# Kernel optimization log

Measured on AMD Instinct MI355X. Metric: run time of the kernel, lower is better.

## Reference

```python
import jax, jax.numpy as jnp
import numpy as np

DIM = 256
NUM_HEADS = 8
SAMPLE_RATIO = 4
B, H, W = 8, 32, 32
HEAD_DIM = DIM // NUM_HEADS
SCALE = HEAD_DIM ** (-0.5)


def conv1x1(x, w, b):
    # x: [B,C,H,W], w: [O,C], b: [O]  (1x1 conv == per-pixel channel matmul)
    return jnp.einsum('bchw,oc->bohw', x, w) + b[None, :, None, None]


def setup_inputs() -> dict:
    key = jax.random.key(0)
    ks = jax.random.split(key, 16)
    s = 0.02
    x = jax.random.normal(ks[0], (B, DIM, H, W), dtype=jnp.float32)
    # gumbel noise for the two gumbel-softmax gates (sampled once, fed as input)
    u_q = jax.random.uniform(ks[1], (B, SAMPLE_RATIO, H, W), minval=1e-6, maxval=1.0 - 1e-6)
    u_k = jax.random.uniform(ks[2], (B, SAMPLE_RATIO, H, W), minval=1e-6, maxval=1.0 - 1e-6)
    g_q = -jnp.log(-jnp.log(u_q))
    g_k = -jnp.log(-jnp.log(u_k))
    return {
        'x': x,
        'g_q': g_q,
        'g_k': g_k,
        'Wsq': jax.random.normal(ks[3], (SAMPLE_RATIO, DIM)) * s,
        'bsq': jnp.zeros((SAMPLE_RATIO,), jnp.float32),
        'Wsk': jax.random.normal(ks[4], (SAMPLE_RATIO, DIM)) * s,
        'bsk': jnp.zeros((SAMPLE_RATIO,), jnp.float32),
        'Wq': jax.random.normal(ks[5], (DIM, DIM)) * s,
        'bq': jnp.zeros((DIM,), jnp.float32),
        'Wk': jax.random.normal(ks[6], (DIM, DIM)) * s,
        'bk': jnp.zeros((DIM,), jnp.float32),
        'Wv': jax.random.normal(ks[7], (DIM, DIM)) * s,
        'bv': jnp.zeros((DIM,), jnp.float32),
        'Wp': jax.random.normal(ks[8], (DIM, DIM)) * s,
        'bp': jnp.zeros((DIM,), jnp.float32),
    }


def reference(x, g_q, g_k, Wsq, bsq, Wsk, bsk, Wq, bq, Wk, bk, Wv, bv, Wp, bp):
    Bn, C, Hh, Ww = x.shape
    N = Hh * Ww
    # gumbel-softmax (soft, tau=1) gates; keep channel 0 only
    sample_q = jax.nn.softmax(conv1x1(x, Wsq, bsq) + g_q, axis=1)[:, :1]   # [B,1,H,W]
    sample_k = jax.nn.softmax(conv1x1(x, Wsk, bsk) + g_k, axis=1)[:, :1]

    q = (sample_q * conv1x1(x, Wq, bq)).reshape(Bn, NUM_HEADS, HEAD_DIM, N)
    k = (sample_k * conv1x1(x, Wk, bk)).reshape(Bn, NUM_HEADS, HEAD_DIM, N)
    v_full = conv1x1(x, Wv, bv)                                            # shortcut [B,C,H,W]
    v = v_full.reshape(Bn, NUM_HEADS, HEAD_DIM, N)

    # dense attention: scores [B,h,N,N]
    attn = jax.nn.softmax(jnp.einsum('bhdn,bhdm->bhnm', q * SCALE, k), axis=-1)
    out = jnp.einsum('bhnm,bhdm->bhdn', attn, v).reshape(Bn, C, Hh, Ww)

    gated = sample_q * out + (1.0 - sample_q) * v_full
    return conv1x1(gated, Wp, bp)
```

## Files before the change

### kernel.cpp

```cpp
#include <hip/hip_runtime.h>
#include <hip/hip_bf16.h>

typedef __hip_bfloat16 bf16;
typedef __attribute__((ext_vector_type(8))) short short8;
typedef __attribute__((ext_vector_type(4))) short sh4;
typedef __attribute__((ext_vector_type(4))) float f32x4;

static __device__ __forceinline__ float bf2f(bf16 h) { return __bfloat162float(h); }
static __device__ __forceinline__ short f2bfs(float f) {
    bf16 h = __float2bfloat16(f);
    return *reinterpret_cast<short*>(&h);
}
static __device__ __forceinline__ short8 cvt8(float4 a, float4 b) {
    short8 o;
    o[0] = f2bfs(a.x); o[1] = f2bfs(a.y); o[2] = f2bfs(a.z); o[3] = f2bfs(a.w);
    o[4] = f2bfs(b.x); o[5] = f2bfs(b.y); o[6] = f2bfs(b.z); o[7] = f2bfs(b.w);
    return o;
}

constexpr int Bn = 8;
constexpr int C  = 256;
constexpr int N  = 1024;
constexpr int NH = 8;
constexpr int HD = 32;
constexpr int TS = 264;
constexpr float SCALE = 0.17677669529663687f;

__global__ __launch_bounds__(256) void k_prep(
    const float* __restrict__ Wq, const float* __restrict__ Wk,
    const float* __restrict__ Wv, const float* __restrict__ Wp,
    bf16* __restrict__ Wb)
{
    const int tid = threadIdx.x;
    const int mat = blockIdx.x >> 2, seg = blockIdx.x & 3;
    const float* src = (mat == 0) ? Wq : (mat == 1) ? Wk : (mat == 2) ? Wv : Wp;
    short* dst = reinterpret_cast<short*>(Wb) + (size_t)mat * 256 * 256;
#pragma unroll
    for (int i = 0; i < 16; ++i) {
        int f4 = seg * 4096 + i * 256 + tid;
        float4 v = reinterpret_cast<const float4*>(src)[f4];
        sh4 o;
        o[0] = f2bfs(v.x); o[1] = f2bfs(v.y); o[2] = f2bfs(v.z); o[3] = f2bfs(v.w);
        *reinterpret_cast<sh4*>(dst + (size_t)f4 * 4) = o;
    }
}

__global__ __launch_bounds__(256) void k_fused5(
    const float* __restrict__ x, const float* __restrict__ gq, const float* __restrict__ gk,
    const float* __restrict__ Wsq, const float* __restrict__ bsq,
    const float* __restrict__ Wsk, const float* __restrict__ bsk,
    const bf16* __restrict__ Wb,
    const float* __restrict__ bq, const float* __restrict__ bk, const float* __restrict__ bv,
    bf16* __restrict__ qo, bf16* __restrict__ ko, bf16* __restrict__ vo,
    float* __restrict__ sqg)
{
    __shared__ short T[64 * TS];
    __shared__ float sq_lds[64];
    __shared__ float sk_lds[64];

    const int tid  = threadIdx.x;
    const int wave = tid >> 6;
    const int lane = tid & 63;
    const int col  = lane & 15;
    const int quad = lane >> 4;

    const int b    = blockIdx.x >> 6;
    const int rest = blockIdx.x & 63;
    const int n0   = (rest >> 2) * 64;
    const int mq   = rest & 3;

    {
        const float* xp = x + (size_t)b * C * N + n0;
        const int row = tid >> 4;
        const int f   = tid & 15;
#pragma unroll
        for (int p = 0; p < 16; ++p) {
            int c = p * 16 + row;
            float4 v = *reinterpret_cast<const float4*>(xp + (size_t)c * N + f * 4);
            T[(f * 4 + 0) * TS + c] = f2bfs(v.x);
            T[(f * 4 + 1) * TS + c] = f2bfs(v.y);
            T[(f * 4 + 2) * TS + c] = f2bfs(v.z);
            T[(f * 4 + 3) * TS + c] = f2bfs(v.w);
        }
    }
    __syncthreads();

    if (wave == 0) {
        const float* wsrc = (col < 4) ? (Wsq + col * C) : (Wsk + (col & 3) * C);
        f32x4 ga[4] = {};
#pragma unroll
        for (int k0 = 0; k0 < 256; k0 += 32) {
            float4 w0 = *reinterpret_cast<const float4*>(wsrc + k0 + quad * 8);
            float4 w1 = *reinterpret_cast<const float4*>(wsrc + k0 + quad * 8 + 4);
            short8 af = cvt8(w0, w1);
#pragma unroll
            for (int cf = 0; cf < 4; ++cf) {
                short8 bfr = *reinterpret_cast<const short8*>(&T[(cf * 16 + col) * TS + k0 + quad * 8]);
                ga[cf] = __builtin_amdgcn_mfma_f32_16x16x32_bf16(af, bfr, ga[cf], 0, 0, 0);
            }
        }
        if (quad < 2) {
            const float* bsrc = (quad == 0) ? bsq : bsk;
            const float* gsrc = (quad == 0) ? gq : gk;
#pragma unroll
            for (int cf = 0; cf < 4; ++cf) {
                int n = n0 + cf * 16 + col;
                float a[4];
#pragma unroll
                for (int r = 0; r < 4; ++r)
                    a[r] = ga[cf][r] + bsrc[r] + gsrc[(size_t)b * 4 * N + (size_t)r * N + n];
                float mx = fmaxf(fmaxf(a[0], a[1]), fmaxf(a[2], a[3]));
                float e = 0.f;
#pragma unroll
                for (int r = 0; r < 4; ++r) e += __expf(a[r] - mx);
                float p0 = __expf(a[0] - mx) / e;
                if (quad == 0) {
                    sq_lds[cf * 16 + col] = p0;
                    if (mq == 0) sqg[b * N + n] = p0;
                } else {
                    sk_lds[cf * 16 + col] = p0;
                }
            }
        }
    }
    __syncthreads();

    const short* Ws = reinterpret_cast<const short*>(Wb);
    const int mbase = mq * 192 + wave * 48;
    f32x4 acc[3][4] = {};
#pragma unroll
    for (int k0 = 0; k0 < 256; k0 += 32) {
        short8 bfr[4];
#pragma unroll
        for (int cf = 0; cf < 4; ++cf)
            bfr[cf] = *reinterpret_cast<const short8*>(&T[(cf * 16 + col) * TS + k0 + quad * 8]);
#pragma unroll
        for (int i = 0; i < 3; ++i) {
            int m = mbase + i * 16;
            const short* wr = Ws + (size_t)(m >> 8) * 65536
                              + (size_t)((m & 255) + col) * 256 + k0 + quad * 8;
            short8 af = *reinterpret_cast<const short8*>(wr);
#pragma unroll
            for (int cf = 0; cf < 4; ++cf)
                acc[i][cf] = __builtin_amdgcn_mfma_f32_16x16x32_bf16(af, bfr[cf], acc[i][cf], 0, 0, 0);
        }
    }
#pragma unroll
    for (int i = 0; i < 3; ++i) {
        int m = mbase + i * 16;
        int mat = m >> 8;
        int cr  = (m & 255) + quad * 4;
        const float* bb = (mat == 0) ? bq : (mat == 1) ? bk : bv;
        float bias[4];
#pragma unroll
        for (int r = 0; r < 4; ++r) bias[r] = bb[cr + r];
        if (mat < 2) {
            short* op = reinterpret_cast<short*>((mat == 0) ? qo : ko) + (size_t)b * N * C;
#pragma unroll
            for (int cf = 0; cf < 4; ++cf) {
                int n = n0 + cf * 16 + col;
                float g = (mat == 0) ? sq_lds[cf * 16 + col] * SCALE
                                     : sk_lds[cf * 16 + col];
                sh4 pack;
#pragma unroll
                for (int r = 0; r < 4; ++r) pack[r] = f2bfs((acc[i][cf][r] + bias[r]) * g);
                *reinterpret_cast<sh4*>(op + (size_t)n * C + cr) = pack;
            }
        } else {
            bf16* op = vo + (size_t)b * C * N;
#pragma unroll
            for (int cf = 0; cf < 4; ++cf) {
                int n = n0 + cf * 16 + col;
#pragma unroll
                for (int r = 0; r < 4; ++r)
                    op[(size_t)(cr + r) * N + n] = __float2bfloat16(acc[i][cf][r] + bias[r]);
            }
        }
    }
}

__global__ __launch_bounds__(256) void k_attn6(
    const bf16* __restrict__ qo, const bf16* __restrict__ ko,
    const bf16* __restrict__ vo, const float* __restrict__ sqg,
    bf16* __restrict__ gt)
{
    __shared__ short P_lds[4][32 * 72];
    __shared__ short K_lds[2][64 * 40];
    __shared__ short V_lds[2][32 * 72];

    const int tid  = threadIdx.x;
    const int wave = tid >> 6;
    const int lane = tid & 63;
    const int col  = lane & 15;
    const int quad = lane >> 4;

    const int b = blockIdx.x >> 6;
    const int h = (blockIdx.x >> 3) & 7;
    const int qbase = (blockIdx.x & 7) * 128 + wave * 32;

    const int skey = tid >> 2;
    const int sd   = (tid & 3) * 8;
    const int svd  = tid >> 3;
    const int svk  = (tid & 7) * 8;

    const short* kgp = reinterpret_cast<const short*>(ko) + (size_t)b * N * C + h * HD;
    const short* vgp = reinterpret_cast<const short*>(vo) + (size_t)b * C * N + (size_t)h * HD * N;
    const short* vp  = vgp;

    short8 qf[2];
    {
        const short* qp = reinterpret_cast<const short*>(qo) + (size_t)b * N * C + h * HD + quad * 8;
#pragma unroll
        for (int g = 0; g < 2; ++g)
            qf[g] = *reinterpret_cast<const short8*>(qp + (size_t)(qbase + g * 16 + col) * C);
    }

    float l[2] = {};
    f32x4 oac[2][2] = {};
    short* P = P_lds[wave];

    short8 kstage = *reinterpret_cast<const short8*>(kgp + (size_t)skey * C + sd);
    short8 vstage = *reinterpret_cast<const short8*>(vgp + (size_t)svd * N + svk);
    *reinterpret_cast<short8*>(&K_lds[0][skey * 40 + sd]) = kstage;
    *reinterpret_cast<short8*>(&V_lds[0][svd * 72 + svk]) = vstage;
    __syncthreads();

    for (int t = 0; t < 16; ++t) {
        const int tn = (t + 1) & 15;
        kstage = *reinterpret_cast<const short8*>(kgp + (size_t)(tn * 64 + skey) * C + sd);
        vstage = *reinterpret_cast<const short8*>(vgp + (size_t)svd * N + tn * 64 + svk);

        const short* Kb = K_lds[t & 1];
        const short* Vb = V_lds[t & 1];

        short8 kf[4];
#pragma unroll
        for (int c = 0; c < 4; ++c)
            kf[c] = *reinterpret_cast<const short8*>(&Kb[(c * 16 + col) * 40 + quad * 8]);

#pragma unroll
        for (int g = 0; g < 2; ++g) {
            float s[16];
#pragma unroll
            for (int c = 0; c < 4; ++c) {
                f32x4 acc = {};
                acc = __builtin_amdgcn_mfma_f32_16x16x32_bf16(kf[c], qf[g], acc, 0, 0, 0);
#pragma unroll
                for (int r = 0; r < 4; ++r) s[c * 4 + r] = acc[r];
            }
            float p[16], lloc = 0.f;
#pragma unroll
            for (int i = 0; i < 16; ++i) { p[i] = __expf(s[i]); lloc += p[i]; }
            lloc += __shfl_xor(lloc, 16, 64);
            lloc += __shfl_xor(lloc, 32, 64);
            l[g] += lloc;
#pragma unroll
            for (int c = 0; c < 4; ++c) {
                sh4 pk;
#pragma unroll
                for (int r = 0; r < 4; ++r) pk[r] = f2bfs(p[c * 4 + r]);
                *reinterpret_cast<sh4*>(&P[(g * 16 + col) * 72 + c * 16 + quad * 4]) = pk;
            }
        }

#pragma unroll
        for (int kg = 0; kg < 2; ++kg) {
            short8 vf[2];
#pragma unroll
            for (int dh = 0; dh < 2; ++dh)
                vf[dh] = *reinterpret_cast<const short8*>(&Vb[(dh * 16 + col) * 72 + kg * 32 + quad * 8]);
#pragma unroll
            for (int g = 0; g < 2; ++g) {
                short8 pf = *reinterpret_cast<const short8*>(&P[(g * 16 + col) * 72 + kg * 32 + quad * 8]);
#pragma unroll
                for (int dh = 0; dh < 2; ++dh)
                    oac[g][dh] = __builtin_amdgcn_mfma_f32_16x16x32_bf16(vf[dh], pf, oac[g][dh], 0, 0, 0);
            }
        }

        *reinterpret_cast<short8*>(&K_lds[(t + 1) & 1][skey * 40 + sd]) = kstage;
        *reinterpret_cast<short8*>(&V_lds[(t + 1) & 1][svd * 72 + svk]) = vstage;
        __syncthreads();
    }

#pragma unroll
    for (int g = 0; g < 2; ++g) {
        const int q = qbase + g * 16 + col;
        const float invl = 1.f / l[g];
        const float sqv  = sqg[b * N + q];
        const float hv   = 1.f - sqv;
        short* gp = reinterpret_cast<short*>(gt) + ((size_t)b * N + q) * C + h * HD + quad * 4;
#pragma unroll
        for (int dh = 0; dh < 2; ++dh) {
            sh4 pack;
#pragma unroll
            for (int r = 0; r < 4; ++r) {
                int d = dh * 16 + quad * 4 + r;
                float vb = bf2f(*reinterpret_cast<const bf16*>(vp + (size_t)d * N + q));
                pack[r] = f2bfs(sqv * (oac[g][dh][r] * invl) + hv * vb);
            }
            *reinterpret_cast<sh4*>(gp + dh * 16) = pack;
        }
    }
}

__global__ __launch_bounds__(256) void k_projm5(
    const bf16* __restrict__ gt, const bf16* __restrict__ Wpb,
    const float* __restrict__ bp, float* __restrict__ out)
{
    __shared__ short G[64 * TS];

    const int tid  = threadIdx.x;
    const int wave = tid >> 6, lane = tid & 63;
    const int col  = lane & 15, quad = lane >> 4;
    const int mrow = blockIdx.x * 64 + wave * 16;
    const int b    = blockIdx.z;
    const int n0   = blockIdx.y * 64;

    {
        const short* gp = reinterpret_cast<const short*>(gt) + ((size_t)b * N + n0) * C;
        const int px = tid >> 2;
        const int c0 = (tid & 3) * 64;
#pragma unroll
        for (int j = 0; j < 8; ++j) {
            short8 v = *reinterpret_cast<const short8*>(gp + (size_t)px * C + c0 + j * 8);
            *reinterpret_cast<short8*>(&G[px * TS + c0 + j * 8]) = v;
        }
    }
    __syncthreads();

    const short* Wm = reinterpret_cast<const short*>(Wpb);

    f32x4 acc[4] = {};
#pragma unroll
    for (int k0 = 0; k0 < 256; k0 += 32) {
        short8 af = *reinterpret_cast<const short8*>(Wm + (size_t)(mrow + col) * 256 + k0 + quad * 8);
#pragma unroll
        for (int cf = 0; cf < 4; ++cf) {
            short8 bfr = *reinterpret_cast<const short8*>(&G[(cf * 16 + col) * TS + k0 + quad * 8]);
            acc[cf] = __builtin_amdgcn_mfma_f32_16x16x32_bf16(af, bfr, acc[cf], 0, 0, 0);
        }
    }

    const int cr = mrow + quad * 4;
    float bias[4];
#pragma unroll
    for (int r = 0; r < 4; ++r) bias[r] = bp[cr + r];
    float* op = out + (size_t)b * C * N;
#pragma unroll
    for (int cf = 0; cf < 4; ++cf) {
        int n = n0 + cf * 16 + col;
#pragma unroll
        for (int r = 0; r < 4; ++r)
            op[(size_t)(cr + r) * N + n] = acc[cf][r] + bias[r];
    }
}

extern "C" void kernel_launch(void* const* d_in, const int* in_sizes, int n_in,
                              void* d_out, int out_size, void* d_ws, size_t ws_size,
                              hipStream_t stream)
{
    const float* x   = (const float*)d_in[0];
    const float* gq  = (const float*)d_in[1];
    const float* gk  = (const float*)d_in[2];
    const float* Wsq = (const float*)d_in[3];
    const float* bsq = (const float*)d_in[4];
    const float* Wsk = (const float*)d_in[5];
    const float* bsk = (const float*)d_in[6];
    const float* Wq  = (const float*)d_in[7];
    const float* bq  = (const float*)d_in[8];
    const float* Wk  = (const float*)d_in[9];
    const float* bk  = (const float*)d_in[10];
    const float* Wv  = (const float*)d_in[11];
    const float* bv  = (const float*)d_in[12];
    const float* Wp  = (const float*)d_in[13];
    const float* bp  = (const float*)d_in[14];

    char* ws = (char*)d_ws;
    float* sqg = (float*)ws;
    bf16* Wb   = (bf16*)(ws + 32768);
    bf16* qo   = (bf16*)(ws + 32768 + 524288);
    bf16* ko   = qo + (size_t)Bn * N * C;
    bf16* vo   = ko + (size_t)Bn * N * C;
    bf16* gt   = vo + (size_t)Bn * C * N;
    float* out = (float*)d_out;

    k_prep<<<16, 256, 0, stream>>>(Wq, Wk, Wv, Wp, Wb);
    k_fused5<<<512, 256, 0, stream>>>(x, gq, gk, Wsq, bsq, Wsk, bsk,
                                      Wb, bq, bk, bv, qo, ko, vo, sqg);
    k_attn6<<<512, 256, 0, stream>>>(qo, ko, vo, sqg, gt);
    k_projm5<<<dim3(4, 16, 8), 256, 0, stream>>>(gt, Wb + 3 * 65536, bp, out);
}
```

Before: 135.5 us.

## Halve attention query tile per wave, double grid, use exp2 with folded log2e

The attention kernel now gives each wave 16 queries instead of 32 and launches 1024 blocks instead of 512. The block index is remapped so that consecutive blocks spread across (batch, head) chunks, which is meant to improve occupancy and cache spread over the 256 CUs. The softmax exponent switches from __expf to exp2f, with log2(e) folded into the Q scaling in the projection kernel. The cost is that every K/V tile is loaded into LDS twice as often per query, raising memory traffic. As before, no max subtraction is done, so this still relies on small logits.

```diff
diff --git a/kernel.cpp b/kernel.cpp
--- a/kernel.cpp
+++ b/kernel.cpp
@@ -1,5 +1,6 @@
 #include <hip/hip_runtime.h>
 #include <hip/hip_bf16.h>
+#include <math.h>
 
 typedef __hip_bfloat16 bf16;
 typedef __attribute__((ext_vector_type(8))) short short8;
@@ -25,6 +26,7 @@
 constexpr int HD = 32;
 constexpr int TS = 264;
 constexpr float SCALE = 0.17677669529663687f;
+constexpr float SCALE_E = 0.17677669529663687f * 1.4426950408889634f;
 
 __global__ __launch_bounds__(256) void k_prep(
     const float* __restrict__ Wq, const float* __restrict__ Wk,
@@ -159,7 +161,7 @@
 #pragma unroll
             for (int cf = 0; cf < 4; ++cf) {
                 int n = n0 + cf * 16 + col;
-                float g = (mat == 0) ? sq_lds[cf * 16 + col] * SCALE
+                float g = (mat == 0) ? sq_lds[cf * 16 + col] * SCALE_E
                                      : sk_lds[cf * 16 + col];
                 sh4 pack;
 #pragma unroll
@@ -184,7 +186,7 @@
     const bf16* __restrict__ vo, const float* __restrict__ sqg,
     bf16* __restrict__ gt)
 {
-    __shared__ short P_lds[4][32 * 72];
+    __shared__ short P_lds[4][16 * 72];
     __shared__ short K_lds[2][64 * 40];
     __shared__ short V_lds[2][32 * 72];
 
@@ -194,9 +196,12 @@
     const int col  = lane & 15;
     const int quad = lane >> 4;
 
-    const int b = blockIdx.x >> 6;
-    const int h = (blockIdx.x >> 3) & 7;
-    const int qbase = (blockIdx.x & 7) * 128 + wave * 32;
+    const int bi    = blockIdx.x;
+    const int chunk = (bi & 7) * 8 + (bi >> 7);
+    const int tile  = (bi >> 3) & 15;
+    const int b = chunk >> 3;
+    const int h = chunk & 7;
+    const int qbase = tile * 64 + wave * 16;
 
     const int skey = tid >> 2;
     const int sd   = (tid & 3) * 8;
@@ -207,16 +212,14 @@
     const short* vgp = reinterpret_cast<const short*>(vo) + (size_t)b * C * N + (size_t)h * HD * N;
     const short* vp  = vgp;
 
-    short8 qf[2];
+    short8 qf;
     {
         const short* qp = reinterpret_cast<const short*>(qo) + (size_t)b * N * C + h * HD + quad * 8;
-#pragma unroll
-        for (int g = 0; g < 2; ++g)
-            qf[g] = *reinterpret_cast<const short8*>(qp + (size_t)(qbase + g * 16 + col) * C);
-    }
-
-    float l[2] = {};
-    f32x4 oac[2][2] = {};
+        qf = *reinterpret_cast<const short8*>(qp + (size_t)(qbase + col) * C);
+    }
+
+    float l = 0.f;
+    f32x4 oac[2] = {};
     short* P = P_lds[wave];
 
     short8 kstage = *reinterpret_cast<const short8*>(kgp + (size_t)skey * C + sd);
@@ -238,28 +241,27 @@
         for (int c = 0; c < 4; ++c)
             kf[c] = *reinterpret_cast<const short8*>(&Kb[(c * 16 + col) * 40 + quad * 8]);
 
-#pragma unroll
-        for (int g = 0; g < 2; ++g) {
+        {
             float s[16];
 #pragma unroll
             for (int c = 0; c < 4; ++c) {
                 f32x4 acc = {};
-                acc = __builtin_amdgcn_mfma_f32_16x16x32_bf16(kf[c], qf[g], acc, 0, 0, 0);
+                acc = __builtin_amdgcn_mfma_f32_16x16x32_bf16(kf[c], qf, acc, 0, 0, 0);
 #pragma unroll
                 for (int r = 0; r < 4; ++r) s[c * 4 + r] = acc[r];
             }
             float p[16], lloc = 0.f;
 #pragma unroll
-            for (int i = 0; i < 16; ++i) { p[i] = __expf(s[i]); lloc += p[i]; }
+            for (int i = 0; i < 16; ++i) { p[i] = exp2f(s[i]); lloc += p[i]; }
             lloc += __shfl_xor(lloc, 16, 64);
             lloc += __shfl_xor(lloc, 32, 64);
-            l[g] += lloc;
+            l += lloc;
 #pragma unroll
             for (int c = 0; c < 4; ++c) {
                 sh4 pk;
 #pragma unroll
                 for (int r = 0; r < 4; ++r) pk[r] = f2bfs(p[c * 4 + r]);
-                *reinterpret_cast<sh4*>(&P[(g * 16 + col) * 72 + c * 16 + quad * 4]) = pk;
+                *reinterpret_cast<sh4*>(&P[col * 72 + c * 16 + quad * 4]) = pk;
             }
         }
 
@@ -269,13 +271,10 @@
 #pragma unroll
             for (int dh = 0; dh < 2; ++dh)
                 vf[dh] = *reinterpret_cast<const short8*>(&Vb[(dh * 16 + col) * 72 + kg * 32 + quad * 8]);
-#pragma unroll
-            for (int g = 0; g < 2; ++g) {
-                short8 pf = *reinterpret_cast<const short8*>(&P[(g * 16 + col) * 72 + kg * 32 + quad * 8]);
-#pragma unroll
-                for (int dh = 0; dh < 2; ++dh)
-                    oac[g][dh] = __builtin_amdgcn_mfma_f32_16x16x32_bf16(vf[dh], pf, oac[g][dh], 0, 0, 0);
-            }
+            short8 pf = *reinterpret_cast<const short8*>(&P[col * 72 + kg * 32 + quad * 8]);
+#pragma unroll
+            for (int dh = 0; dh < 2; ++dh)
+                oac[dh] = __builtin_amdgcn_mfma_f32_16x16x32_bf16(vf[dh], pf, oac[dh], 0, 0, 0);
         }
 
         *reinterpret_cast<short8*>(&K_lds[(t + 1) & 1][skey * 40 + sd]) = kstage;
@@ -283,10 +282,9 @@
         __syncthreads();
     }
 
-#pragma unroll
-    for (int g = 0; g < 2; ++g) {
-        const int q = qbase + g * 16 + col;
-        const float invl = 1.f / l[g];
+    {
+        const int q = qbase + col;
+        const float invl = 1.f / l;
         const float sqv  = sqg[b * N + q];
         const float hv   = 1.f - sqv;
         short* gp = reinterpret_cast<short*>(gt) + ((size_t)b * N + q) * C + h * HD + quad * 4;
@@ -297,7 +295,7 @@
             for (int r = 0; r < 4; ++r) {
                 int d = dh * 16 + quad * 4 + r;
                 float vb = bf2f(*reinterpret_cast<const bf16*>(vp + (size_t)d * N + q));
-                pack[r] = f2bfs(sqv * (oac[g][dh][r] * invl) + hv * vb);
+                pack[r] = f2bfs(sqv * (oac[dh][r] * invl) + hv * vb);
             }
             *reinterpret_cast<sh4*>(gp + dh * 16) = pack;
         }
@@ -388,6 +386,6 @@
     k_prep<<<16, 256, 0, stream>>>(Wq, Wk, Wv, Wp, Wb);
     k_fused5<<<512, 256, 0, stream>>>(x, gq, gk, Wsq, bsq, Wsk, bsk,
                                       Wb, bq, bk, bv, qo, ko, vo, sqg);
-    k_attn6<<<512, 256, 0, stream>>>(qo, ko, vo, sqg, gt);
+    k_attn6<<<1024, 256, 0, stream>>>(qo, ko, vo, sqg, gt);
     k_projm5<<<dim3(4, 16, 8), 256, 0, stream>>>(gt, Wb + 3 * 65536, bp, out);
 }
```

Measured after the change: 137.7 us. About the same (+1.6%).

## Fuse all stages into one cooperative kernel with grid syncs

Applied to the files above, without the earlier changes.

Replaces the four separate launches (weight prep, QKV projection, attention, output projection) with one cooperative kernel that separates the stages with grid.sync(), and keeps the old launches as a fallback if the cooperative launch fails. The aim is to remove per-launch overhead and the idle gaps between kernels. It also folds log2(e) into the query scale so the softmax can use exp2f instead of __expf. Risks include the cost of grid-wide barriers, occupancy limits from launch_bounds(256,2) needed for 512 co-resident blocks, and the fallback running if co-residency cannot be guaranteed.

```diff
diff --git a/kernel.cpp b/kernel.cpp
--- a/kernel.cpp
+++ b/kernel.cpp
@@ -1,5 +1,9 @@
 #include <hip/hip_runtime.h>
 #include <hip/hip_bf16.h>
+#include <hip/hip_cooperative_groups.h>
+#include <math.h>
+
+namespace cg = cooperative_groups;
 
 typedef __hip_bfloat16 bf16;
 typedef __attribute__((ext_vector_type(8))) short short8;
@@ -25,6 +29,324 @@
 constexpr int HD = 32;
 constexpr int TS = 264;
 constexpr float SCALE = 0.17677669529663687f;
+constexpr float SCALE_E = 0.17677669529663687f * 1.4426950408889634f;
+
+__global__ __launch_bounds__(256, 2) void k_all(
+    const float* __restrict__ x, const float* __restrict__ gq, const float* __restrict__ gk,
+    const float* __restrict__ Wsq, const float* __restrict__ bsq,
+    const float* __restrict__ Wsk, const float* __restrict__ bsk,
+    const float* __restrict__ Wq, const float* __restrict__ bq,
+    const float* __restrict__ Wk, const float* __restrict__ bk,
+    const float* __restrict__ Wv, const float* __restrict__ bv,
+    const float* __restrict__ Wp, const float* __restrict__ bp,
+    bf16* __restrict__ Wb, bf16* __restrict__ qo, bf16* __restrict__ ko,
+    bf16* __restrict__ vo, bf16* __restrict__ gt, float* __restrict__ sqg,
+    float* __restrict__ out)
+{
+    __shared__ __align__(16) char smem[37888];
+    cg::grid_group grid = cg::this_grid();
+
+    const int tid  = threadIdx.x;
+    const int bid  = blockIdx.x;
+    const int wave = tid >> 6;
+    const int lane = tid & 63;
+    const int col  = lane & 15;
+    const int quad = lane >> 4;
+
+    if (bid < 256) {
+        int idx = bid * 256 + tid;
+        int mat = idx >> 14;
+        const float* src = (mat == 0) ? Wq : (mat == 1) ? Wk : (mat == 2) ? Wv : Wp;
+        float4 v = reinterpret_cast<const float4*>(src)[idx & 16383];
+        sh4 o;
+        o[0] = f2bfs(v.x); o[1] = f2bfs(v.y); o[2] = f2bfs(v.z); o[3] = f2bfs(v.w);
+        reinterpret_cast<sh4*>(reinterpret_cast<short*>(Wb))[idx] = o;
+    }
+    grid.sync();
+
+    {
+        short* T      = reinterpret_cast<short*>(smem);
+        float* sq_lds = reinterpret_cast<float*>(smem + 33792);
+        float* sk_lds = sq_lds + 64;
+
+        const int b    = bid >> 6;
+        const int rest = bid & 63;
+        const int n0   = (rest >> 2) * 64;
+        const int mq   = rest & 3;
+
+        {
+            const float* xp = x + (size_t)b * C * N + n0;
+            const int row = tid >> 4;
+            const int f   = tid & 15;
+#pragma unroll
+            for (int p = 0; p < 16; ++p) {
+                int c = p * 16 + row;
+                float4 v = *reinterpret_cast<const float4*>(xp + (size_t)c * N + f * 4);
+                T[(f * 4 + 0) * TS + c] = f2bfs(v.x);
+                T[(f * 4 + 1) * TS + c] = f2bfs(v.y);
+                T[(f * 4 + 2) * TS + c] = f2bfs(v.z);
+                T[(f * 4 + 3) * TS + c] = f2bfs(v.w);
+            }
+        }
+        __syncthreads();
+
+        if (wave == 0) {
+            const float* wsrc = (col < 4) ? (Wsq + col * C) : (Wsk + (col & 3) * C);
+            f32x4 ga[4] = {};
+#pragma unroll
+            for (int k0 = 0; k0 < 256; k0 += 32) {
+                float4 w0 = *reinterpret_cast<const float4*>(wsrc + k0 + quad * 8);
+                float4 w1 = *reinterpret_cast<const float4*>(wsrc + k0 + quad * 8 + 4);
+                short8 af = cvt8(w0, w1);
+#pragma unroll
+                for (int cf = 0; cf < 4; ++cf) {
+                    short8 bfr = *reinterpret_cast<const short8*>(&T[(cf * 16 + col) * TS + k0 + quad * 8]);
+                    ga[cf] = __builtin_amdgcn_mfma_f32_16x16x32_bf16(af, bfr, ga[cf], 0, 0, 0);
+                }
+            }
+            if (quad < 2) {
+                const float* bsrc = (quad == 0) ? bsq : bsk;
+                const float* gsrc = (quad == 0) ? gq : gk;
+#pragma unroll
+                for (int cf = 0; cf < 4; ++cf) {
+                    int n = n0 + cf * 16 + col;
+                    float a[4];
+#pragma unroll
+                    for (int r = 0; r < 4; ++r)
+                        a[r] = ga[cf][r] + bsrc[r] + gsrc[(size_t)b * 4 * N + (size_t)r * N + n];
+                    float mx = fmaxf(fmaxf(a[0], a[1]), fmaxf(a[2], a[3]));
+                    float e = 0.f;
+#pragma unroll
+                    for (int r = 0; r < 4; ++r) e += __expf(a[r] - mx);
+                    float p0 = __expf(a[0] - mx) / e;
+                    if (quad == 0) {
+                        sq_lds[cf * 16 + col] = p0;
+                        if (mq == 0) sqg[b * N + n] = p0;
+                    } else {
+                        sk_lds[cf * 16 + col] = p0;
+                    }
+                }
+            }
+        }
+        __syncthreads();
+
+        const short* Ws = reinterpret_cast<const short*>(Wb);
+        const int mbase = mq * 192 + wave * 48;
+        f32x4 acc[3][4] = {};
+#pragma unroll
+        for (int k0 = 0; k0 < 256; k0 += 32) {
+            short8 bfr[4];
+#pragma unroll
+            for (int cf = 0; cf < 4; ++cf)
+                bfr[cf] = *reinterpret_cast<const short8*>(&T[(cf * 16 + col) * TS + k0 + quad * 8]);
+#pragma unroll
+            for (int i = 0; i < 3; ++i) {
+                int m = mbase + i * 16;
+                const short* wr = Ws + (size_t)(m >> 8) * 65536
+                                  + (size_t)((m & 255) + col) * 256 + k0 + quad * 8;
+                short8 af = *reinterpret_cast<const short8*>(wr);
+#pragma unroll
+                for (int cf = 0; cf < 4; ++cf)
+                    acc[i][cf] = __builtin_amdgcn_mfma_f32_16x16x32_bf16(af, bfr[cf], acc[i][cf], 0, 0, 0);
+            }
+        }
+#pragma unroll
+        for (int i = 0; i < 3; ++i) {
+            int m = mbase + i * 16;
+            int mat = m >> 8;
+            int cr  = (m & 255) + quad * 4;
+            const float* bb = (mat == 0) ? bq : (mat == 1) ? bk : bv;
+            float bias[4];
+#pragma unroll
+            for (int r = 0; r < 4; ++r) bias[r] = bb[cr + r];
+            if (mat < 2) {
+                short* op = reinterpret_cast<short*>((mat == 0) ? qo : ko) + (size_t)b * N * C;
+#pragma unroll
+                for (int cf = 0; cf < 4; ++cf) {
+                    int n = n0 + cf * 16 + col;
+                    float g = (mat == 0) ? sq_lds[cf * 16 + col] * SCALE_E
+                                         : sk_lds[cf * 16 + col];
+                    sh4 pack;
+#pragma unroll
+                    for (int r = 0; r < 4; ++r) pack[r] = f2bfs((acc[i][cf][r] + bias[r]) * g);
+                    *reinterpret_cast<sh4*>(op + (size_t)n * C + cr) = pack;
+                }
+            } else {
+                bf16* op = vo + (size_t)b * C * N;
+#pragma unroll
+                for (int cf = 0; cf < 4; ++cf) {
+                    int n = n0 + cf * 16 + col;
+#pragma unroll
+                    for (int r = 0; r < 4; ++r)
+                        op[(size_t)(cr + r) * N + n] = __float2bfloat16(acc[i][cf][r] + bias[r]);
+                }
+            }
+        }
+    }
+    grid.sync();
+
+    {
+        short* Pb  = reinterpret_cast<short*>(smem);
+        short* Kb0 = Pb + 9216;
+        short* Vb0 = Pb + 14336;
+
+        const int b = bid >> 6;
+        const int h = (bid >> 3) & 7;
+        const int qbase = (bid & 7) * 128 + wave * 32;
+
+        const int skey = tid >> 2;
+        const int sd   = (tid & 3) * 8;
+        const int svd  = tid >> 3;
+        const int svk  = (tid & 7) * 8;
+
+        const short* kgp = reinterpret_cast<const short*>(ko) + (size_t)b * N * C + h * HD;
+        const short* vgp = reinterpret_cast<const short*>(vo) + (size_t)b * C * N + (size_t)h * HD * N;
+        const short* vp  = vgp;
+
+        short8 qf[2];
+        {
+            const short* qp = reinterpret_cast<const short*>(qo) + (size_t)b * N * C + h * HD + quad * 8;
+#pragma unroll
+            for (int g = 0; g < 2; ++g)
+                qf[g] = *reinterpret_cast<const short8*>(qp + (size_t)(qbase + g * 16 + col) * C);
+        }
+
+        float l[2] = {};
+        f32x4 oac[2][2] = {};
+        short* P = Pb + wave * 2304;
+
+        short8 kstage = *reinterpret_cast<const short8*>(kgp + (size_t)skey * C + sd);
+        short8 vstage = *reinterpret_cast<const short8*>(vgp + (size_t)svd * N + svk);
+        *reinterpret_cast<short8*>(&Kb0[skey * 40 + sd]) = kstage;
+        *reinterpret_cast<short8*>(&Vb0[svd * 72 + svk]) = vstage;
+        __syncthreads();
+
+        for (int t = 0; t < 16; ++t) {
+            const int tn = (t + 1) & 15;
+            kstage = *reinterpret_cast<const short8*>(kgp + (size_t)(tn * 64 + skey) * C + sd);
+            vstage = *reinterpret_cast<const short8*>(vgp + (size_t)svd * N + tn * 64 + svk);
+
+            const short* Kb = Kb0 + (t & 1) * 2560;
+            const short* Vb = Vb0 + (t & 1) * 2304;
+
+            short8 kf[4];
+#pragma unroll
+            for (int c = 0; c < 4; ++c)
+                kf[c] = *reinterpret_cast<const short8*>(&Kb[(c * 16 + col) * 40 + quad * 8]);
+
+#pragma unroll
+            for (int g = 0; g < 2; ++g) {
+                float s[16];
+#pragma unroll
+                for (int c = 0; c < 4; ++c) {
+                    f32x4 acc = {};
+                    acc = __builtin_amdgcn_mfma_f32_16x16x32_bf16(kf[c], qf[g], acc, 0, 0, 0);
+#pragma unroll
+                    for (int r = 0; r < 4; ++r) s[c * 4 + r] = acc[r];
+                }
+                float p[16], lloc = 0.f;
+#pragma unroll
+                for (int i = 0; i < 16; ++i) { p[i] = exp2f(s[i]); lloc += p[i]; }
+                lloc += __shfl_xor(lloc, 16, 64);
+                lloc += __shfl_xor(lloc, 32, 64);
+                l[g] += lloc;
+#pragma unroll
+                for (int c = 0; c < 4; ++c) {
+                    sh4 pk;
+#pragma unroll
+                    for (int r = 0; r < 4; ++r) pk[r] = f2bfs(p[c * 4 + r]);
+                    *reinterpret_cast<sh4*>(&P[(g * 16 + col) * 72 + c * 16 + quad * 4]) = pk;
+                }
+            }
+
+#pragma unroll
+            for (int kg = 0; kg < 2; ++kg) {
+                short8 vf[2];
+#pragma unroll
+                for (int dh = 0; dh < 2; ++dh)
+                    vf[dh] = *reinterpret_cast<const short8*>(&Vb[(dh * 16 + col) * 72 + kg * 32 + quad * 8]);
+#pragma unroll
+                for (int g = 0; g < 2; ++g) {
+                    short8 pf = *reinterpret_cast<const short8*>(&P[(g * 16 + col) * 72 + kg * 32 + quad * 8]);
+#pragma unroll
+                    for (int dh = 0; dh < 2; ++dh)
+                        oac[g][dh] = __builtin_amdgcn_mfma_f32_16x16x32_bf16(vf[dh], pf, oac[g][dh], 0, 0, 0);
+                }
+            }
+
+            *reinterpret_cast<short8*>(&Kb0[((t + 1) & 1) * 2560 + skey * 40 + sd]) = kstage;
+            *reinterpret_cast<short8*>(&Vb0[((t + 1) & 1) * 2304 + svd * 72 + svk]) = vstage;
+            __syncthreads();
+        }
+
+#pragma unroll
+        for (int g = 0; g < 2; ++g) {
+            const int q = qbase + g * 16 + col;
+            const float invl = 1.f / l[g];
+            const float sqv  = sqg[b * N + q];
+            const float hv   = 1.f - sqv;
+            short* gp = reinterpret_cast<short*>(gt) + ((size_t)b * N + q) * C + h * HD + quad * 4;
+#pragma unroll
+            for (int dh = 0; dh < 2; ++dh) {
+                sh4 pack;
+#pragma unroll
+                for (int r = 0; r < 4; ++r) {
+                    int d = dh * 16 + quad * 4 + r;
+                    float vb = bf2f(*reinterpret_cast<const bf16*>(vp + (size_t)d * N + q));
+                    pack[r] = f2bfs(sqv * (oac[g][dh][r] * invl) + hv * vb);
+                }
+                *reinterpret_cast<sh4*>(gp + dh * 16) = pack;
+            }
+        }
+    }
+    grid.sync();
+
+    {
+        short* G = reinterpret_cast<short*>(smem);
+
+        const int mrow = (bid & 3) * 64 + wave * 16;
+        const int n0   = ((bid >> 2) & 15) * 64;
+        const int b    = bid >> 6;
+
+        {
+            const short* gp = reinterpret_cast<const short*>(gt) + ((size_t)b * N + n0) * C;
+            const int px = tid >> 2;
+            const int c0 = (tid & 3) * 64;
+#pragma unroll
+            for (int j = 0; j < 8; ++j) {
+                short8 v = *reinterpret_cast<const short8*>(gp + (size_t)px * C + c0 + j * 8);
+                *reinterpret_cast<short8*>(&G[px * TS + c0 + j * 8]) = v;
+            }
+        }
+        __syncthreads();
+
+        const short* Wm = reinterpret_cast<const short*>(Wb) + 3 * 65536;
+
+        f32x4 acc[4] = {};
+#pragma unroll
+        for (int k0 = 0; k0 < 256; k0 += 32) {
+            short8 af = *reinterpret_cast<const short8*>(Wm + (size_t)(mrow + col) * 256 + k0 + quad * 8);
+#pragma unroll
+            for (int cf = 0; cf < 4; ++cf) {
+                short8 bfr = *reinterpret_cast<const short8*>(&G[(cf * 16 + col) * TS + k0 + quad * 8]);
+                acc[cf] = __builtin_amdgcn_mfma_f32_16x16x32_bf16(af, bfr, acc[cf], 0, 0, 0);
+            }
+        }
+
+        const int cr = mrow + quad * 4;
+        float bias[4];
+#pragma unroll
+        for (int r = 0; r < 4; ++r) bias[r] = bp[cr + r];
+        float* op = out + (size_t)b * C * N;
+#pragma unroll
+        for (int cf = 0; cf < 4; ++cf) {
+            int n = n0 + cf * 16 + col;
+#pragma unroll
+            for (int r = 0; r < 4; ++r)
+                op[(size_t)(cr + r) * N + n] = acc[cf][r] + bias[r];
+        }
+    }
+}
 
 __global__ __launch_bounds__(256) void k_prep(
     const float* __restrict__ Wq, const float* __restrict__ Wk,
@@ -159,7 +481,7 @@
 #pragma unroll
             for (int cf = 0; cf < 4; ++cf) {
                 int n = n0 + cf * 16 + col;
-                float g = (mat == 0) ? sq_lds[cf * 16 + col] * SCALE
+                float g = (mat == 0) ? sq_lds[cf * 16 + col] * SCALE_E
                                      : sk_lds[cf * 16 + col];
                 sh4 pack;
 #pragma unroll
@@ -250,7 +572,7 @@
             }
             float p[16], lloc = 0.f;
 #pragma unroll
-            for (int i = 0; i < 16; ++i) { p[i] = __expf(s[i]); lloc += p[i]; }
+            for (int i = 0; i < 16; ++i) { p[i] = exp2f(s[i]); lloc += p[i]; }
             lloc += __shfl_xor(lloc, 16, 64);
             lloc += __shfl_xor(lloc, 32, 64);
             l[g] += lloc;
@@ -385,9 +707,18 @@
     bf16* gt   = vo + (size_t)Bn * C * N;
     float* out = (float*)d_out;
 
-    k_prep<<<16, 256, 0, stream>>>(Wq, Wk, Wv, Wp, Wb);
-    k_fused5<<<512, 256, 0, stream>>>(x, gq, gk, Wsq, bsq, Wsk, bsk,
-                                      Wb, bq, bk, bv, qo, ko, vo, sqg);
-    k_attn6<<<512, 256, 0, stream>>>(qo, ko, vo, sqg, gt);
-    k_projm5<<<dim3(4, 16, 8), 256, 0, stream>>>(gt, Wb + 3 * 65536, bp, out);
+    void* args[] = { (void*)&x, (void*)&gq, (void*)&gk, (void*)&Wsq, (void*)&bsq,
+                     (void*)&Wsk, (void*)&bsk, (void*)&Wq, (void*)&bq, (void*)&Wk,
+                     (void*)&bk, (void*)&Wv, (void*)&bv, (void*)&Wp, (void*)&bp,
+                     (void*)&Wb, (void*)&qo, (void*)&ko, (void*)&vo, (void*)&gt,
+                     (void*)&sqg, (void*)&out };
+    hipError_t err = hipLaunchCooperativeKernel(reinterpret_cast<const void*>(k_all),
+                                                dim3(512), dim3(256), args, 0, stream);
+    if (err != hipSuccess) {
+        k_prep<<<16, 256, 0, stream>>>(Wq, Wk, Wv, Wp, Wb);
+        k_fused5<<<512, 256, 0, stream>>>(x, gq, gk, Wsq, bsq, Wsk, bsk,
+                                          Wb, bq, bk, bv, qo, ko, vo, sqg);
+        k_attn6<<<512, 256, 0, stream>>>(qo, ko, vo, sqg, gt);
+        k_projm5<<<dim3(4, 16, 8), 256, 0, stream>>>(gt, Wb + 3 * 65536, bp, out);
+    }
 }
```

New measurement: 321.7 us. 2.37x slower.

## Fold log2e into Q scale, remap attention blocks per XCD, widen weight prep

Applied to the files above, without the earlier changes.

The attention score scale now includes log2(e), so the softmax exponent can use exp2f instead of __expf. Attention block indices are remapped so that all query tiles of one (batch, head) land on the same XCD, which is meant to improve L2 reuse of that head's K and V. The weight-conversion prep kernel is spread over 256 blocks with one float4 per thread instead of 16 blocks each looping over 16. The risks are small rounding differences in the exponent, and the remap depends on the hardware assigning blocks to XCDs round-robin.

```diff
diff --git a/kernel.cpp b/kernel.cpp
--- a/kernel.cpp
+++ b/kernel.cpp
@@ -1,5 +1,6 @@
 #include <hip/hip_runtime.h>
 #include <hip/hip_bf16.h>
+#include <math.h>
 
 typedef __hip_bfloat16 bf16;
 typedef __attribute__((ext_vector_type(8))) short short8;
@@ -24,25 +25,20 @@
 constexpr int NH = 8;
 constexpr int HD = 32;
 constexpr int TS = 264;
-constexpr float SCALE = 0.17677669529663687f;
+constexpr float SCALE_E = 0.17677669529663687f * 1.4426950408889634f;
 
 __global__ __launch_bounds__(256) void k_prep(
     const float* __restrict__ Wq, const float* __restrict__ Wk,
     const float* __restrict__ Wv, const float* __restrict__ Wp,
     bf16* __restrict__ Wb)
 {
-    const int tid = threadIdx.x;
-    const int mat = blockIdx.x >> 2, seg = blockIdx.x & 3;
+    const int idx = blockIdx.x * 256 + threadIdx.x;
+    const int mat = idx >> 14;
     const float* src = (mat == 0) ? Wq : (mat == 1) ? Wk : (mat == 2) ? Wv : Wp;
-    short* dst = reinterpret_cast<short*>(Wb) + (size_t)mat * 256 * 256;
-#pragma unroll
-    for (int i = 0; i < 16; ++i) {
-        int f4 = seg * 4096 + i * 256 + tid;
-        float4 v = reinterpret_cast<const float4*>(src)[f4];
-        sh4 o;
-        o[0] = f2bfs(v.x); o[1] = f2bfs(v.y); o[2] = f2bfs(v.z); o[3] = f2bfs(v.w);
-        *reinterpret_cast<sh4*>(dst + (size_t)f4 * 4) = o;
-    }
+    float4 v = reinterpret_cast<const float4*>(src)[idx & 16383];
+    sh4 o;
+    o[0] = f2bfs(v.x); o[1] = f2bfs(v.y); o[2] = f2bfs(v.z); o[3] = f2bfs(v.w);
+    reinterpret_cast<sh4*>(reinterpret_cast<short*>(Wb))[idx] = o;
 }
 
 __global__ __launch_bounds__(256) void k_fused5(
@@ -159,7 +155,7 @@
 #pragma unroll
             for (int cf = 0; cf < 4; ++cf) {
                 int n = n0 + cf * 16 + col;
-                float g = (mat == 0) ? sq_lds[cf * 16 + col] * SCALE
+                float g = (mat == 0) ? sq_lds[cf * 16 + col] * SCALE_E
                                      : sk_lds[cf * 16 + col];
                 sh4 pack;
 #pragma unroll
@@ -194,9 +190,14 @@
     const int col  = lane & 15;
     const int quad = lane >> 4;
 
-    const int b = blockIdx.x >> 6;
-    const int h = (blockIdx.x >> 3) & 7;
-    const int qbase = (blockIdx.x & 7) * 128 + wave * 32;
+    const int bid   = blockIdx.x;
+    const int xcd   = bid & 7;
+    const int idx   = bid >> 3;
+    const int chunk = xcd * 8 + (idx >> 3);
+    const int qt    = idx & 7;
+    const int b = chunk >> 3;
+    const int h = chunk & 7;
+    const int qbase = qt * 128 + wave * 32;
 
     const int skey = tid >> 2;
     const int sd   = (tid & 3) * 8;
@@ -250,7 +251,7 @@
             }
             float p[16], lloc = 0.f;
 #pragma unroll
-            for (int i = 0; i < 16; ++i) { p[i] = __expf(s[i]); lloc += p[i]; }
+            for (int i = 0; i < 16; ++i) { p[i] = exp2f(s[i]); lloc += p[i]; }
             lloc += __shfl_xor(lloc, 16, 64);
             lloc += __shfl_xor(lloc, 32, 64);
             l[g] += lloc;
@@ -385,7 +386,7 @@
     bf16* gt   = vo + (size_t)Bn * C * N;
     float* out = (float*)d_out;
 
-    k_prep<<<16, 256, 0, stream>>>(Wq, Wk, Wv, Wp, Wb);
+    k_prep<<<256, 256, 0, stream>>>(Wq, Wk, Wv, Wp, Wb);
     k_fused5<<<512, 256, 0, stream>>>(x, gq, gk, Wsq, bsq, Wsk, bsk,
                                       Wb, bq, bk, bv, qo, ko, vo, sqg);
     k_attn6<<<512, 256, 0, stream>>>(qo, ko, vo, sqg, gt);
```

Measured after the change: 142.3 us. 1.05x slower.
